# Optimization experiments

Measured on AMD Instinct MI355X. Metric: run time of the kernel, lower is better.

Reference implementation:

```python
import jax, jax.numpy as jnp
import numpy as np

THRESH = 0.3
OUT_THRESH = 0.3
LENS = 0.5  # surrogate-gradient window (ActFun in snn-delays repo)


@jax.custom_vjp
def spike(x):
    # Heaviside spike with rectangular surrogate gradient
    return (x > 0.0).astype(x.dtype)

def _spike_fwd(x):
    return spike(x), x

def _spike_bwd(x, g):
    return (g * (jnp.abs(x) < LENS).astype(g.dtype),)

spike.defvjp(_spike_fwd, _spike_bwd)


def setup_inputs() -> dict:
    key = jax.random.key(0)
    ks = jax.random.split(key, 7)
    B, T, I, H, O = 256, 50, 1024, 2048, 20
    # binary input spikes (rate ~0.2), as an SNN would receive
    inp = (jax.random.uniform(ks[0], (B, T, I)) < 0.2).astype(jnp.float32)
    # Linear(in, out, bias=False) -> weight [out, in], Kaiming-uniform-ish init
    w_ih = jax.random.uniform(ks[1], (H, I), minval=-1.0, maxval=1.0) / np.sqrt(I)
    w_hh = jax.random.uniform(ks[2], (H, H), minval=-1.0, maxval=1.0) / np.sqrt(H)
    w_ho = jax.random.uniform(ks[3], (O, H), minval=-1.0, maxval=1.0) / np.sqrt(H)
    tau_m_h = 0.83 + 0.1 * jax.random.normal(ks[4], (H,))
    tau_m_o = 0.83 + 0.1 * jax.random.normal(ks[5], (O,))
    return {"input": inp, "w_ih": w_ih, "w_hh": w_hh, "w_ho": w_ho,
            "tau_m_h": tau_m_h, "tau_m_o": tau_m_o}


def _rsnn_forward(inp, w_ih, w_hh, w_ho, tau_m_h, tau_m_o):
    B, T, I = inp.shape
    H = w_ih.shape[0]
    O = w_ho.shape[0]
    alpha_h = jnp.exp(-1.0 / tau_m_h)  # [H]
    alpha_o = jnp.exp(-1.0 / tau_m_o)  # [O]
    zH = jnp.zeros((B, H), inp.dtype)
    zO = jnp.zeros((B, O), inp.dtype)

    def step(carry, x_t):
        h_mem, h_spk, o_mem, o_spk, o_sum, mot = carry
        # hidden membrane update: input + recurrent + decayed (reset-gated) mem
        h_mem = (x_t @ w_ih.T) + (h_spk @ w_hh.T) + h_mem * alpha_h * (1.0 - h_spk)
        h_spk = spike(h_mem - THRESH)
        # output membrane update
        o_mem = o_mem * alpha_o * (1.0 - o_spk) + h_spk @ w_ho.T
        o_spk = spike(o_mem - OUT_THRESH)
        o_sum = o_sum + o_spk
        mot = mot + jax.nn.softmax(o_mem, axis=1)
        return (h_mem, h_spk, o_mem, o_spk, o_sum, mot), None

    init = (zH, zH, zO, zO, zO, zO)
    (h_mem, h_spk, o_mem, o_spk, o_sum, mot), _ = jax.lax.scan(
        step, init, jnp.swapaxes(inp, 0, 1))  # scan over time [T,B,I]
    return o_sum / T, mot


def reference(input, w_ih, w_hh, w_ho, tau_m_h, tau_m_o):
    return _rsnn_forward(input, w_ih, w_hh, w_ho, tau_m_h, tau_m_o)
```

## Files before the change

### kernel.cpp

```cpp
#include <hip/hip_runtime.h>
#include <stdint.h>
#include <math.h>


#define B_   256
#define T_   50
#define I_   1024
#define H_   2048
#define O_   20
#define XIN_T  262144
#define XS_BUF 524288
#define WNT 294912
#define WPL 98304

typedef __attribute__((ext_vector_type(4))) int intx4;
typedef long long ll_t;

__device__ __forceinline__ int digit_of(float v, int p) {
  int W = (int)rintf(v * 134217728.0f);
  int c0 = ((W + 128) & 255) - 128;
  int W1 = (W - c0) >> 8;
  int c1 = ((W1 + 128) & 255) - 128;
  int W2 = (W1 - c1) >> 8;
  return (p == 0) ? c0 : (p == 1) ? c1 : W2;
}

__global__ void prep_w(const float* __restrict__ w_ih,
                       const float* __restrict__ w_hh,
                       int8_t* __restrict__ Wtl) {
  int blk = blockIdx.x;
  int n = blk / 9, kg = blk % 9;
  int k9 = (kg * 256 + (int)threadIdx.x) * 4;
  int p = k9 / 3072, kk = k9 % 3072;
  const float* src = (kk < 1024) ? (w_ih + n * I_ + kk)
                                 : (w_hh + n * H_ + (kk - 1024));
  float4 v = *(const float4*)src;
  int d0 = digit_of(v.x, p) & 255;
  int d1 = digit_of(v.y, p) & 255;
  int d2 = digit_of(v.z, p) & 255;
  int d3 = digit_of(v.w, p) & 255;
  int packed = d0 | (d1 << 8) | (d2 << 16) | (d3 << 24);
  size_t off = (size_t)(n >> 5) * WNT + (size_t)p * WPL + (kk >> 6) * 2048 +
               (n & 31) * 64 + (kk & 63);
  *(int*)(Wtl + off) = packed;
}

__global__ void init_k(int8_t* __restrict__ Xin, int8_t* __restrict__ Xs,
                       float* __restrict__ Hm, const float* __restrict__ input,
                       const float* __restrict__ tau_h,
                       const float* __restrict__ tau_o,
                       float* __restrict__ AlphaH, float* __restrict__ AlphaO,
                       const float* __restrict__ w_ho, double* __restrict__ WhoD,
                       float* __restrict__ Om, float* __restrict__ Osp,
                       float* __restrict__ Osu, float* __restrict__ Mo) {
  int id = blockIdx.x * 256 + threadIdx.x;
  {
    int b = id >> 8, i4 = (id & 255) * 4;
    for (int t = 0; t < T_; ++t) {
      float4 v = *(const float4*)(input + ((size_t)(b * T_ + t) << 10) + i4);
      uchar4 pk;
      pk.x = v.x > 0.5f ? 1 : 0;
      pk.y = v.y > 0.5f ? 1 : 0;
      pk.z = v.z > 0.5f ? 1 : 0;
      pk.w = v.w > 0.5f ? 1 : 0;
      *(uchar4*)(Xin + (size_t)t * XIN_T + (b >> 6) * 65536 + (i4 >> 6) * 4096 +
                 (b & 63) * 64 + (i4 & 63)) = pk;
    }
  }
  *(double*)(Xs + (size_t)id * 8) = 0.0;
  *(float4*)(Hm + (size_t)id * 8) = make_float4(0.f, 0.f, 0.f, 0.f);
  *(float4*)(Hm + (size_t)id * 8 + 4) = make_float4(0.f, 0.f, 0.f, 0.f);
  if (id < 64 * O_ * 32) {
    int nt = id / 640, rem = id % 640, o = rem / 32, hl = rem & 31;
    WhoD[id] = (double)w_ho[o * H_ + nt * 32 + hl];
  }
  if (id < H_) AlphaH[id] = (float)exp((double)(-1.0f / tau_h[id]));
  if (id < O_) AlphaO[id] = (float)exp((double)(-1.0f / tau_o[id]));
  if (id < B_ * O_) {
    Om[id] = 0.f; Osp[id] = 0.f; Osu[id] = 0.f; Mo[id] = 0.f;
  }
}

__global__ __launch_bounds__(512, 2) void step_k(
    const int8_t* __restrict__ Wtl, const int8_t* __restrict__ Xin,
    int8_t* __restrict__ Xs, float* __restrict__ Hm, double* __restrict__ Po,
    const double* __restrict__ WhoD, const float* __restrict__ AlphaH,
    const float* __restrict__ AlphaO, float* __restrict__ Om,
    float* __restrict__ Osp, float* __restrict__ Osu, float* __restrict__ Mo,
    int t) {
  __shared__ double WhoL[640];
  __shared__ __align__(16) int8_t red[98304];
  __shared__ int8_t spk_lT[2048];

  const int j = blockIdx.x;
  const int nt = (j & 7) * 8 + ((j >> 3) & 7);
  const int mg = j >> 6;
  const int tid = threadIdx.x;
  const int l = tid & 63, k = tid >> 6;
  const int r_ = l & 15, q = l >> 4;

  for (int i = tid; i < 640; i += 512) WhoL[i] = WhoD[nt * 640 + i];

  const int8_t* Ain = Xin + (size_t)t * XIN_T + mg * 65536 + r_ * 64 + q * 16;
  const int8_t* Asp = Xs + (size_t)(t & 1) * XS_BUF + mg * 131072 + r_ * 64 + q * 16;
  const int8_t* Bw = Wtl + (size_t)nt * WNT + r_ * 64 + q * 16;
  const int u0 = k * 6;

  intx4 acc[4][2][3];
#pragma unroll
  for (int fr = 0; fr < 4; ++fr)
#pragma unroll
    for (int fc = 0; fc < 2; ++fc)
#pragma unroll
      for (int p = 0; p < 3; ++p) acc[fr][fc][p] = (intx4){0, 0, 0, 0};

  intx4 a[2][4], b[2][2][3];
  {
    const int8_t* ap = (u0 < 16) ? (Ain + u0 * 4096) : (Asp + (u0 - 16) * 4096);
#pragma unroll
    for (int fr = 0; fr < 4; ++fr) a[0][fr] = *(const intx4*)(ap + fr * 1024);
    const int8_t* bp = Bw + u0 * 2048;
#pragma unroll
    for (int p = 0; p < 3; ++p)
#pragma unroll
      for (int fc = 0; fc < 2; ++fc)
        b[0][fc][p] = *(const intx4*)(bp + p * WPL + fc * 1024);
  }
#pragma unroll
  for (int i = 0; i < 6; ++i) {
    const int cur = i & 1, nxt = cur ^ 1;
    if (i < 5) {
      const int un = u0 + i + 1;
      const int8_t* ap = (un < 16) ? (Ain + un * 4096) : (Asp + (un - 16) * 4096);
#pragma unroll
      for (int fr = 0; fr < 4; ++fr) a[nxt][fr] = *(const intx4*)(ap + fr * 1024);
      const int8_t* bp = Bw + un * 2048;
#pragma unroll
      for (int p = 0; p < 3; ++p)
#pragma unroll
        for (int fc = 0; fc < 2; ++fc)
          b[nxt][fc][p] = *(const intx4*)(bp + p * WPL + fc * 1024);
    }
#pragma unroll
    for (int fr = 0; fr < 4; ++fr)
#pragma unroll
      for (int fc = 0; fc < 2; ++fc)
#pragma unroll
        for (int p = 0; p < 3; ++p)
          acc[fr][fc][p] = __builtin_amdgcn_mfma_i32_16x16x64_i8(
              a[cur][fr], b[cur][fc][p], acc[fr][fc][p], 0, 0, 0);
  }

#define REDP(w, idx) (red + (((w) * 12 + (idx)) * 64 + l) * 16)

  int8_t* Xw = Xs + (size_t)((t + 1) & 1) * XS_BUF;
  auto epilogue = [&](intx4 s0, intx4 s1, intx4 s2, int fr_e, int fc_e) {
    const int h = nt * 32 + fc_e * 16 + r_;
    const float alpha = AlphaH[h];
    unsigned spkpack = 0;
#pragma unroll
    for (int jj = 0; jj < 4; ++jj) {
      ll_t Sv = (ll_t)s0[jj] + ((ll_t)s1[jj] << 8) + ((ll_t)s2[jj] << 16);
      float M = (float)((double)Sv * 7.450580596923828125e-9);
      const int brl = fr_e * 16 + q * 4 + jj;
      const int idx = (mg * 64 + brl) * H_ + h;
      float hp = Hm[idx];
      float spf = (hp - 0.3f) > 0.f ? 1.f : 0.f;
      float hm = M + hp * alpha * (1.0f - spf);
      Hm[idx] = hm;
      unsigned spk = (hm - 0.3f) > 0.f ? 1u : 0u;
      Xw[mg * 131072 + (h >> 6) * 4096 + brl * 64 + (h & 63)] = (int8_t)spk;
      spkpack |= spk << (8 * jj);
    }
    *(unsigned*)(spk_lT + (fc_e * 16 + r_) * 64 + fr_e * 16 + q * 4) = spkpack;
  };

#pragma unroll
  for (int fr = 0; fr < 2; ++fr)
#pragma unroll
    for (int fc = 0; fc < 2; ++fc)
#pragma unroll
      for (int p = 0; p < 3; ++p)
        *(intx4*)REDP(k, (fr * 2 + fc) * 3 + p) = acc[fr][fc][p];
  __syncthreads();
  if (k < 4) {
    const int fr_e = k >> 1, fc_e = k & 1;
    const int base = (fr_e * 2 + fc_e) * 3;
    intx4 s0 = (intx4){0, 0, 0, 0}, s1 = s0, s2 = s0;
#pragma unroll
    for (int w = 0; w < 8; ++w) {
      s0 = s0 + *(const intx4*)REDP(w, base + 0);
      s1 = s1 + *(const intx4*)REDP(w, base + 1);
      s2 = s2 + *(const intx4*)REDP(w, base + 2);
    }
    epilogue(s0, s1, s2, fr_e, fc_e);
  }
  __syncthreads();
#pragma unroll
  for (int fr = 0; fr < 2; ++fr)
#pragma unroll
    for (int fc = 0; fc < 2; ++fc)
#pragma unroll
      for (int p = 0; p < 3; ++p)
        *(intx4*)REDP(k, (fr * 2 + fc) * 3 + p) = acc[2 + fr][fc][p];
  __syncthreads();
  if (k >= 4) {
    const int fr_e = 2 + ((k - 4) >> 1), fc_e = k & 1;
    const int base = ((fr_e - 2) * 2 + fc_e) * 3;
    intx4 s0 = (intx4){0, 0, 0, 0}, s1 = s0, s2 = s0;
#pragma unroll
    for (int w = 0; w < 8; ++w) {
      s0 = s0 + *(const intx4*)REDP(w, base + 0);
      s1 = s1 + *(const intx4*)REDP(w, base + 1);
      s2 = s2 + *(const intx4*)REDP(w, base + 2);
    }
    epilogue(s0, s1, s2, fr_e, fc_e);
  }
  __syncthreads();

  if (tid < 256) {
    const int bl = tid >> 2, og = (tid & 3) * 5;
    const double* W0 = WhoL + og * 32;
    double a0 = 0, a1 = 0, a2 = 0, a3 = 0, a4 = 0;
#pragma unroll
    for (int hl = 0; hl < 32; ++hl) {
      double m = (double)spk_lT[hl * 64 + bl];
      a0 += m * W0[hl];
      a1 += m * W0[32 + hl];
      a2 += m * W0[64 + hl];
      a3 += m * W0[96 + hl];
      a4 += m * W0[128 + hl];
    }
    double* dst =
        Po + ((size_t)((t & 1) * 256 + mg * 64 + bl) * 64 + nt) * 20 + og;
    dst[0] = a0; dst[1] = a1; dst[2] = a2; dst[3] = a3; dst[4] = a4;
  } else if (k == 7 && t > 0) {
    float m = -3.0e38f;
    if (l < 20) {
      const double* pp = Po + ((size_t)(((t - 1) & 1) * 256 + j) * 64) * 20 + l;
      double s = 0.0;
#pragma unroll
      for (int n2 = 0; n2 < 64; ++n2) s += pp[n2 * 20];
      m = Om[j * O_ + l] * AlphaO[l] * (1.0f - Osp[j * O_ + l]) + (float)s;
    }
    float mx = m;
#pragma unroll
    for (int off = 16; off > 0; off >>= 1)
      mx = fmaxf(mx, __shfl_xor(mx, off, 32));
    float eo = (l < 20) ? expf(m - mx) : 0.f;
    float se = eo;
#pragma unroll
    for (int off = 16; off > 0; off >>= 1) se += __shfl_xor(se, off, 32);
    if (l < 20) {
      float sp = (m - 0.3f) > 0.f ? 1.f : 0.f;
      Om[j * O_ + l] = m;
      Osp[j * O_ + l] = sp;
      Osu[j * O_ + l] += sp;
      Mo[j * O_ + l] += eo / se;
    }
  }
#undef REDP
}

__global__ void final_k(const double* __restrict__ Po,
                        const float* __restrict__ AlphaO,
                        const float* __restrict__ Om,
                        const float* __restrict__ Osp,
                        const float* __restrict__ Osu,
                        const float* __restrict__ Mo, float* __restrict__ out) {
  __shared__ float om_l[O_];
  const int j = blockIdx.x, tid = threadIdx.x;
  if (tid < O_) {
    const double* pp = Po + ((size_t)(256 + j) * 64) * 20 + tid;
    double s = 0.0;
#pragma unroll
    for (int n2 = 0; n2 < 64; ++n2) s += pp[n2 * 20];
    float r = (float)s;
    float m = Om[j * O_ + tid] * AlphaO[tid] * (1.0f - Osp[j * O_ + tid]) + r;
    om_l[tid] = m;
  }
  __syncthreads();
  if (tid < O_) {
    float m = om_l[tid];
    float mx = om_l[0];
#pragma unroll
    for (int o = 1; o < O_; ++o) mx = fmaxf(mx, om_l[o]);
    float se = 0.f;
#pragma unroll
    for (int o = 0; o < O_; ++o) se += expf(om_l[o] - mx);
    float sp = (m - 0.3f) > 0.f ? 1.f : 0.f;
    out[j * O_ + tid] = (Osu[j * O_ + tid] + sp) / 50.0f;
    out[B_ * O_ + j * O_ + tid] = Mo[j * O_ + tid] + expf(m - mx) / se;
  }
}

extern "C" void kernel_launch(void* const* d_in, const int* in_sizes, int n_in,
                              void* d_out, int out_size, void* d_ws, size_t ws_size,
                              hipStream_t stream) {
  const float* input = (const float*)d_in[0];
  const float* w_ih  = (const float*)d_in[1];
  const float* w_hh  = (const float*)d_in[2];
  const float* w_ho  = (const float*)d_in[3];
  const float* tau_h = (const float*)d_in[4];
  const float* tau_o = (const float*)d_in[5];

  char* ws = (char*)d_ws;
  int8_t* Wtl    = (int8_t*)(ws);
  int8_t* Xin    = (int8_t*)(ws + 18874368);
  int8_t* Xs     = (int8_t*)(ws + 31981568);
  double* Po     = (double*)(ws + 33030144);
  float*  Hm     = (float*)(ws + 38273024);
  double* WhoD   = (double*)(ws + 40370176);
  float*  AlphaH = (float*)(ws + 40697856);
  float*  AlphaO = (float*)(ws + 40706048);
  float*  Om     = (float*)(ws + 40706176);
  float*  Osp    = (float*)(ws + 40726656);
  float*  Osu    = (float*)(ws + 40747136);
  float*  Mo     = (float*)(ws + 40767616);
  float*  out    = (float*)d_out;

  prep_w<<<2048 * 9, 256, 0, stream>>>(w_ih, w_hh, Wtl);
  init_k<<<256, 256, 0, stream>>>(Xin, Xs, Hm, input, tau_h, tau_o, AlphaH,
                                  AlphaO, w_ho, WhoD, Om, Osp, Osu, Mo);
  for (int t = 0; t < T_; ++t) {
    step_k<<<256, 512, 0, stream>>>(Wtl, Xin, Xs, Hm, Po, WhoD, AlphaH, AlphaO,
                                    Om, Osp, Osu, Mo, t);
  }
  final_k<<<256, 64, 0, stream>>>(Po, AlphaO, Om, Osp, Osu, Mo, out);
}
```

Baseline: 900.8 us.

## Fuse all timesteps into one persistent cooperative kernel with register-resident state

Replaces the 50 per-timestep launches and the final kernel with a single cooperative kernel that loops over time and uses grid.sync between steps. Each block keeps its weight slice in registers for the whole run (breg) and holds the hidden membrane and output state in registers instead of global memory, which removes the per-step weight reloads and the Hm/Om round trips. In exchange it pays a grid-wide barrier per step and much higher register pressure, which could cause spills or lower occupancy, and it requires all 256 blocks to be resident at once.

After: 3.207 ms. 3.56x slower.

```diff
diff --git a/kernel.cpp b/kernel.cpp
--- a/kernel.cpp
+++ b/kernel.cpp
@@ -1,6 +1,9 @@
 #include <hip/hip_runtime.h>
+#include <hip/hip_cooperative_groups.h>
 #include <stdint.h>
 #include <math.h>
+
+namespace cg = cooperative_groups;
 
 
 #define B_   256
@@ -46,13 +49,12 @@
 }
 
 __global__ void init_k(int8_t* __restrict__ Xin, int8_t* __restrict__ Xs,
-                       float* __restrict__ Hm, const float* __restrict__ input,
+                       const float* __restrict__ input,
                        const float* __restrict__ tau_h,
                        const float* __restrict__ tau_o,
                        float* __restrict__ AlphaH, float* __restrict__ AlphaO,
-                       const float* __restrict__ w_ho, double* __restrict__ WhoD,
-                       float* __restrict__ Om, float* __restrict__ Osp,
-                       float* __restrict__ Osu, float* __restrict__ Mo) {
+                       const float* __restrict__ w_ho,
+                       double* __restrict__ WhoD) {
   int id = blockIdx.x * 256 + threadIdx.x;
   {
     int b = id >> 8, i4 = (id & 255) * 4;
@@ -68,26 +70,20 @@
     }
   }
   *(double*)(Xs + (size_t)id * 8) = 0.0;
-  *(float4*)(Hm + (size_t)id * 8) = make_float4(0.f, 0.f, 0.f, 0.f);
-  *(float4*)(Hm + (size_t)id * 8 + 4) = make_float4(0.f, 0.f, 0.f, 0.f);
   if (id < 64 * O_ * 32) {
     int nt = id / 640, rem = id % 640, o = rem / 32, hl = rem & 31;
     WhoD[id] = (double)w_ho[o * H_ + nt * 32 + hl];
   }
   if (id < H_) AlphaH[id] = (float)exp((double)(-1.0f / tau_h[id]));
   if (id < O_) AlphaO[id] = (float)exp((double)(-1.0f / tau_o[id]));
-  if (id < B_ * O_) {
-    Om[id] = 0.f; Osp[id] = 0.f; Osu[id] = 0.f; Mo[id] = 0.f;
-  }
-}
-
-__global__ __launch_bounds__(512, 2) void step_k(
+}
+
+__global__ __launch_bounds__(512, 2) void rsnn_k(
     const int8_t* __restrict__ Wtl, const int8_t* __restrict__ Xin,
-    int8_t* __restrict__ Xs, float* __restrict__ Hm, double* __restrict__ Po,
+    int8_t* __restrict__ Xs, double* __restrict__ Po,
     const double* __restrict__ WhoD, const float* __restrict__ AlphaH,
-    const float* __restrict__ AlphaO, float* __restrict__ Om,
-    float* __restrict__ Osp, float* __restrict__ Osu, float* __restrict__ Mo,
-    int t) {
+    const float* __restrict__ AlphaO, float* __restrict__ out) {
+  cg::grid_group grid = cg::this_grid();
   __shared__ double WhoL[640];
   __shared__ __align__(16) int8_t red[98304];
   __shared__ int8_t spk_lT[2048];
@@ -101,197 +97,181 @@
 
   for (int i = tid; i < 640; i += 512) WhoL[i] = WhoD[nt * 640 + i];
 
-  const int8_t* Ain = Xin + (size_t)t * XIN_T + mg * 65536 + r_ * 64 + q * 16;
-  const int8_t* Asp = Xs + (size_t)(t & 1) * XS_BUF + mg * 131072 + r_ * 64 + q * 16;
+  const int fr_e = (k < 4) ? (k >> 1) : (2 + ((k - 4) >> 1));
+  const int fc_e = k & 1;
+  const int h_e = nt * 32 + fc_e * 16 + r_;
+  const float alpha_e = AlphaH[h_e];
+  const float alphaO_r = (l < O_) ? AlphaO[l] : 0.f;
+
+  float hm[4] = {0.f, 0.f, 0.f, 0.f};
+  float om = 0.f, osp = 0.f, osu = 0.f, mo = 0.f;
+
+  const int u0 = k * 6;
   const int8_t* Bw = Wtl + (size_t)nt * WNT + r_ * 64 + q * 16;
-  const int u0 = k * 6;
-
-  intx4 acc[4][2][3];
-#pragma unroll
-  for (int fr = 0; fr < 4; ++fr)
-#pragma unroll
-    for (int fc = 0; fc < 2; ++fc)
-#pragma unroll
-      for (int p = 0; p < 3; ++p) acc[fr][fc][p] = (intx4){0, 0, 0, 0};
-
-  intx4 a[2][4], b[2][2][3];
-  {
-    const int8_t* ap = (u0 < 16) ? (Ain + u0 * 4096) : (Asp + (u0 - 16) * 4096);
-#pragma unroll
-    for (int fr = 0; fr < 4; ++fr) a[0][fr] = *(const intx4*)(ap + fr * 1024);
-    const int8_t* bp = Bw + u0 * 2048;
+  intx4 breg[6][2][3];
+#pragma unroll
+  for (int i = 0; i < 6; ++i)
 #pragma unroll
     for (int p = 0; p < 3; ++p)
 #pragma unroll
       for (int fc = 0; fc < 2; ++fc)
-        b[0][fc][p] = *(const intx4*)(bp + p * WPL + fc * 1024);
-  }
-#pragma unroll
-  for (int i = 0; i < 6; ++i) {
-    const int cur = i & 1, nxt = cur ^ 1;
-    if (i < 5) {
-      const int un = u0 + i + 1;
-      const int8_t* ap = (un < 16) ? (Ain + un * 4096) : (Asp + (un - 16) * 4096);
-#pragma unroll
-      for (int fr = 0; fr < 4; ++fr) a[nxt][fr] = *(const intx4*)(ap + fr * 1024);
-      const int8_t* bp = Bw + un * 2048;
-#pragma unroll
-      for (int p = 0; p < 3; ++p)
+        breg[i][fc][p] =
+            *(const intx4*)(Bw + (size_t)(u0 + i) * 2048 + p * WPL + fc * 1024);
+
+  const int arow = r_ * 64 + q * 16;
+
+#define REDP(w, idx) (red + (((w) * 12 + (idx)) * 64 + l) * 16)
+
+  for (int t = 0; t <= T_; ++t) {
+    grid.sync();
+
+    if (t < T_) {
+      const int8_t* Ain = Xin + (size_t)t * XIN_T + mg * 65536 + arow;
+      const int8_t* Asp = Xs + (size_t)(t & 1) * XS_BUF + mg * 131072 + arow;
+      int8_t* Xw = Xs + (size_t)((t + 1) & 1) * XS_BUF;
+
+      intx4 acc[4][2][3];
+#pragma unroll
+      for (int fr = 0; fr < 4; ++fr)
 #pragma unroll
         for (int fc = 0; fc < 2; ++fc)
-          b[nxt][fc][p] = *(const intx4*)(bp + p * WPL + fc * 1024);
+#pragma unroll
+          for (int p = 0; p < 3; ++p) acc[fr][fc][p] = (intx4){0, 0, 0, 0};
+
+#pragma unroll
+      for (int i = 0; i < 6; ++i) {
+        const int u = u0 + i;
+        const int8_t* ap =
+            (u < 16) ? (Ain + u * 4096) : (Asp + (u - 16) * 4096);
+        intx4 a0 = *(const intx4*)ap;
+        intx4 a1 = *(const intx4*)(ap + 1024);
+        intx4 a2 = *(const intx4*)(ap + 2048);
+        intx4 a3 = *(const intx4*)(ap + 3072);
+#pragma unroll
+        for (int p = 0; p < 3; ++p)
+#pragma unroll
+          for (int fc = 0; fc < 2; ++fc) {
+            acc[0][fc][p] = __builtin_amdgcn_mfma_i32_16x16x64_i8(
+                a0, breg[i][fc][p], acc[0][fc][p], 0, 0, 0);
+            acc[1][fc][p] = __builtin_amdgcn_mfma_i32_16x16x64_i8(
+                a1, breg[i][fc][p], acc[1][fc][p], 0, 0, 0);
+            acc[2][fc][p] = __builtin_amdgcn_mfma_i32_16x16x64_i8(
+                a2, breg[i][fc][p], acc[2][fc][p], 0, 0, 0);
+            acc[3][fc][p] = __builtin_amdgcn_mfma_i32_16x16x64_i8(
+                a3, breg[i][fc][p], acc[3][fc][p], 0, 0, 0);
+          }
+      }
+
+      auto epilogue = [&](intx4 s0, intx4 s1, intx4 s2) {
+        unsigned spkpack = 0;
+#pragma unroll
+        for (int jj = 0; jj < 4; ++jj) {
+          ll_t Sv = (ll_t)s0[jj] + ((ll_t)s1[jj] << 8) + ((ll_t)s2[jj] << 16);
+          float M = (float)((double)Sv * 7.450580596923828125e-9);
+          float hp = hm[jj];
+          float spf = (hp - 0.3f) > 0.f ? 1.f : 0.f;
+          float hmn = M + hp * alpha_e * (1.0f - spf);
+          hm[jj] = hmn;
+          unsigned spk = (hmn - 0.3f) > 0.f ? 1u : 0u;
+          const int brl = fr_e * 16 + q * 4 + jj;
+          Xw[mg * 131072 + (h_e >> 6) * 4096 + brl * 64 + (h_e & 63)] =
+              (int8_t)spk;
+          spkpack |= spk << (8 * jj);
+        }
+        *(unsigned*)(spk_lT + (fc_e * 16 + r_) * 64 + fr_e * 16 + q * 4) =
+            spkpack;
+      };
+
+#pragma unroll
+      for (int fr = 0; fr < 2; ++fr)
+#pragma unroll
+        for (int fc = 0; fc < 2; ++fc)
+#pragma unroll
+          for (int p = 0; p < 3; ++p)
+            *(intx4*)REDP(k, (fr * 2 + fc) * 3 + p) = acc[fr][fc][p];
+      __syncthreads();
+      if (k < 4) {
+        const int base = (fr_e * 2 + fc_e) * 3;
+        intx4 s0 = (intx4){0, 0, 0, 0}, s1 = s0, s2 = s0;
+#pragma unroll
+        for (int w = 0; w < 8; ++w) {
+          s0 = s0 + *(const intx4*)REDP(w, base + 0);
+          s1 = s1 + *(const intx4*)REDP(w, base + 1);
+          s2 = s2 + *(const intx4*)REDP(w, base + 2);
+        }
+        epilogue(s0, s1, s2);
+      }
+      __syncthreads();
+#pragma unroll
+      for (int fr = 0; fr < 2; ++fr)
+#pragma unroll
+        for (int fc = 0; fc < 2; ++fc)
+#pragma unroll
+          for (int p = 0; p < 3; ++p)
+            *(intx4*)REDP(k, (fr * 2 + fc) * 3 + p) = acc[2 + fr][fc][p];
+      __syncthreads();
+      if (k >= 4) {
+        const int base = ((fr_e - 2) * 2 + fc_e) * 3;
+        intx4 s0 = (intx4){0, 0, 0, 0}, s1 = s0, s2 = s0;
+#pragma unroll
+        for (int w = 0; w < 8; ++w) {
+          s0 = s0 + *(const intx4*)REDP(w, base + 0);
+          s1 = s1 + *(const intx4*)REDP(w, base + 1);
+          s2 = s2 + *(const intx4*)REDP(w, base + 2);
+        }
+        epilogue(s0, s1, s2);
+      }
+      __syncthreads();
+
+      if (tid < 256) {
+        const int bl = tid >> 2, og = (tid & 3) * 5;
+        const double* W0 = WhoL + og * 32;
+        double a0 = 0, a1 = 0, a2 = 0, a3 = 0, a4 = 0;
+#pragma unroll
+        for (int hl = 0; hl < 32; ++hl) {
+          double m = (double)spk_lT[hl * 64 + bl];
+          a0 += m * W0[hl];
+          a1 += m * W0[32 + hl];
+          a2 += m * W0[64 + hl];
+          a3 += m * W0[96 + hl];
+          a4 += m * W0[128 + hl];
+        }
+        double* dst =
+            Po + ((size_t)((t & 1) * 256 + mg * 64 + bl) * 64 + nt) * 20 + og;
+        dst[0] = a0; dst[1] = a1; dst[2] = a2; dst[3] = a3; dst[4] = a4;
+      }
     }
-#pragma unroll
-    for (int fr = 0; fr < 4; ++fr)
-#pragma unroll
-      for (int fc = 0; fc < 2; ++fc)
-#pragma unroll
-        for (int p = 0; p < 3; ++p)
-          acc[fr][fc][p] = __builtin_amdgcn_mfma_i32_16x16x64_i8(
-              a[cur][fr], b[cur][fc][p], acc[fr][fc][p], 0, 0, 0);
-  }
-
-#define REDP(w, idx) (red + (((w) * 12 + (idx)) * 64 + l) * 16)
-
-  int8_t* Xw = Xs + (size_t)((t + 1) & 1) * XS_BUF;
-  auto epilogue = [&](intx4 s0, intx4 s1, intx4 s2, int fr_e, int fc_e) {
-    const int h = nt * 32 + fc_e * 16 + r_;
-    const float alpha = AlphaH[h];
-    unsigned spkpack = 0;
-#pragma unroll
-    for (int jj = 0; jj < 4; ++jj) {
-      ll_t Sv = (ll_t)s0[jj] + ((ll_t)s1[jj] << 8) + ((ll_t)s2[jj] << 16);
-      float M = (float)((double)Sv * 7.450580596923828125e-9);
-      const int brl = fr_e * 16 + q * 4 + jj;
-      const int idx = (mg * 64 + brl) * H_ + h;
-      float hp = Hm[idx];
-      float spf = (hp - 0.3f) > 0.f ? 1.f : 0.f;
-      float hm = M + hp * alpha * (1.0f - spf);
-      Hm[idx] = hm;
-      unsigned spk = (hm - 0.3f) > 0.f ? 1u : 0u;
-      Xw[mg * 131072 + (h >> 6) * 4096 + brl * 64 + (h & 63)] = (int8_t)spk;
-      spkpack |= spk << (8 * jj);
-    }
-    *(unsigned*)(spk_lT + (fc_e * 16 + r_) * 64 + fr_e * 16 + q * 4) = spkpack;
-  };
-
-#pragma unroll
-  for (int fr = 0; fr < 2; ++fr)
-#pragma unroll
-    for (int fc = 0; fc < 2; ++fc)
-#pragma unroll
-      for (int p = 0; p < 3; ++p)
-        *(intx4*)REDP(k, (fr * 2 + fc) * 3 + p) = acc[fr][fc][p];
-  __syncthreads();
-  if (k < 4) {
-    const int fr_e = k >> 1, fc_e = k & 1;
-    const int base = (fr_e * 2 + fc_e) * 3;
-    intx4 s0 = (intx4){0, 0, 0, 0}, s1 = s0, s2 = s0;
-#pragma unroll
-    for (int w = 0; w < 8; ++w) {
-      s0 = s0 + *(const intx4*)REDP(w, base + 0);
-      s1 = s1 + *(const intx4*)REDP(w, base + 1);
-      s2 = s2 + *(const intx4*)REDP(w, base + 2);
-    }
-    epilogue(s0, s1, s2, fr_e, fc_e);
-  }
-  __syncthreads();
-#pragma unroll
-  for (int fr = 0; fr < 2; ++fr)
-#pragma unroll
-    for (int fc = 0; fc < 2; ++fc)
-#pragma unroll
-      for (int p = 0; p < 3; ++p)
-        *(intx4*)REDP(k, (fr * 2 + fc) * 3 + p) = acc[2 + fr][fc][p];
-  __syncthreads();
-  if (k >= 4) {
-    const int fr_e = 2 + ((k - 4) >> 1), fc_e = k & 1;
-    const int base = ((fr_e - 2) * 2 + fc_e) * 3;
-    intx4 s0 = (intx4){0, 0, 0, 0}, s1 = s0, s2 = s0;
-#pragma unroll
-    for (int w = 0; w < 8; ++w) {
-      s0 = s0 + *(const intx4*)REDP(w, base + 0);
-      s1 = s1 + *(const intx4*)REDP(w, base + 1);
-      s2 = s2 + *(const intx4*)REDP(w, base + 2);
-    }
-    epilogue(s0, s1, s2, fr_e, fc_e);
-  }
-  __syncthreads();
-
-  if (tid < 256) {
-    const int bl = tid >> 2, og = (tid & 3) * 5;
-    const double* W0 = WhoL + og * 32;
-    double a0 = 0, a1 = 0, a2 = 0, a3 = 0, a4 = 0;
-#pragma unroll
-    for (int hl = 0; hl < 32; ++hl) {
-      double m = (double)spk_lT[hl * 64 + bl];
-      a0 += m * W0[hl];
-      a1 += m * W0[32 + hl];
-      a2 += m * W0[64 + hl];
-      a3 += m * W0[96 + hl];
-      a4 += m * W0[128 + hl];
-    }
-    double* dst =
-        Po + ((size_t)((t & 1) * 256 + mg * 64 + bl) * 64 + nt) * 20 + og;
-    dst[0] = a0; dst[1] = a1; dst[2] = a2; dst[3] = a3; dst[4] = a4;
-  } else if (k == 7 && t > 0) {
-    float m = -3.0e38f;
-    if (l < 20) {
-      const double* pp = Po + ((size_t)(((t - 1) & 1) * 256 + j) * 64) * 20 + l;
-      double s = 0.0;
-#pragma unroll
-      for (int n2 = 0; n2 < 64; ++n2) s += pp[n2 * 20];
-      m = Om[j * O_ + l] * AlphaO[l] * (1.0f - Osp[j * O_ + l]) + (float)s;
-    }
-    float mx = m;
-#pragma unroll
-    for (int off = 16; off > 0; off >>= 1)
-      mx = fmaxf(mx, __shfl_xor(mx, off, 32));
-    float eo = (l < 20) ? expf(m - mx) : 0.f;
-    float se = eo;
-#pragma unroll
-    for (int off = 16; off > 0; off >>= 1) se += __shfl_xor(se, off, 32);
-    if (l < 20) {
-      float sp = (m - 0.3f) > 0.f ? 1.f : 0.f;
-      Om[j * O_ + l] = m;
-      Osp[j * O_ + l] = sp;
-      Osu[j * O_ + l] += sp;
-      Mo[j * O_ + l] += eo / se;
+
+    if (k == 7 && t > 0) {
+      float m = -3.0e38f;
+      if (l < O_) {
+        const double* pp =
+            Po + ((size_t)(((t - 1) & 1) * 256 + j) * 64) * 20 + l;
+        double s = 0.0;
+#pragma unroll
+        for (int n2 = 0; n2 < 64; ++n2) s += pp[n2 * 20];
+        m = om * alphaO_r * (1.0f - osp) + (float)s;
+      }
+      float mx = m;
+#pragma unroll
+      for (int off = 16; off > 0; off >>= 1)
+        mx = fmaxf(mx, __shfl_xor(mx, off, 32));
+      float eo = (l < O_) ? expf(m - mx) : 0.f;
+      float se = eo;
+#pragma unroll
+      for (int off = 16; off > 0; off >>= 1) se += __shfl_xor(se, off, 32);
+      if (l < O_) {
+        float sp = (m - 0.3f) > 0.f ? 1.f : 0.f;
+        if (t < T_) {
+          om = m; osp = sp; osu += sp; mo += eo / se;
+        } else {
+          out[j * O_ + l] = (osu + sp) / 50.0f;
+          out[B_ * O_ + j * O_ + l] = mo + eo / se;
+        }
+      }
     }
   }
 #undef REDP
-}
-
-__global__ void final_k(const double* __restrict__ Po,
-                        const float* __restrict__ AlphaO,
-                        const float* __restrict__ Om,
-                        const float* __restrict__ Osp,
-                        const float* __restrict__ Osu,
-                        const float* __restrict__ Mo, float* __restrict__ out) {
-  __shared__ float om_l[O_];
-  const int j = blockIdx.x, tid = threadIdx.x;
-  if (tid < O_) {
-    const double* pp = Po + ((size_t)(256 + j) * 64) * 20 + tid;
-    double s = 0.0;
-#pragma unroll
-    for (int n2 = 0; n2 < 64; ++n2) s += pp[n2 * 20];
-    float r = (float)s;
-    float m = Om[j * O_ + tid] * AlphaO[tid] * (1.0f - Osp[j * O_ + tid]) + r;
-    om_l[tid] = m;
-  }
-  __syncthreads();
-  if (tid < O_) {
-    float m = om_l[tid];
-    float mx = om_l[0];
-#pragma unroll
-    for (int o = 1; o < O_; ++o) mx = fmaxf(mx, om_l[o]);
-    float se = 0.f;
-#pragma unroll
-    for (int o = 0; o < O_; ++o) se += expf(om_l[o] - mx);
-    float sp = (m - 0.3f) > 0.f ? 1.f : 0.f;
-    out[j * O_ + tid] = (Osu[j * O_ + tid] + sp) / 50.0f;
-    out[B_ * O_ + j * O_ + tid] = Mo[j * O_ + tid] + expf(m - mx) / se;
-  }
 }
 
 extern "C" void kernel_launch(void* const* d_in, const int* in_sizes, int n_in,
@@ -309,22 +289,16 @@
   int8_t* Xin    = (int8_t*)(ws + 18874368);
   int8_t* Xs     = (int8_t*)(ws + 31981568);
   double* Po     = (double*)(ws + 33030144);
-  float*  Hm     = (float*)(ws + 38273024);
   double* WhoD   = (double*)(ws + 40370176);
   float*  AlphaH = (float*)(ws + 40697856);
   float*  AlphaO = (float*)(ws + 40706048);
-  float*  Om     = (float*)(ws + 40706176);
-  float*  Osp    = (float*)(ws + 40726656);
-  float*  Osu    = (float*)(ws + 40747136);
-  float*  Mo     = (float*)(ws + 40767616);
   float*  out    = (float*)d_out;
 
   prep_w<<<2048 * 9, 256, 0, stream>>>(w_ih, w_hh, Wtl);
-  init_k<<<256, 256, 0, stream>>>(Xin, Xs, Hm, input, tau_h, tau_o, AlphaH,
-                                  AlphaO, w_ho, WhoD, Om, Osp, Osu, Mo);
-  for (int t = 0; t < T_; ++t) {
-    step_k<<<256, 512, 0, stream>>>(Wtl, Xin, Xs, Hm, Po, WhoD, AlphaH, AlphaO,
-                                    Om, Osp, Osu, Mo, t);
-  }
-  final_k<<<256, 64, 0, stream>>>(Po, AlphaO, Om, Osp, Osu, Mo, out);
-}
+  init_k<<<256, 256, 0, stream>>>(Xin, Xs, input, tau_h, tau_o, AlphaH,
+                                  AlphaO, w_ho, WhoD);
+  void* args[] = {(void*)&Wtl, (void*)&Xin, (void*)&Xs, (void*)&Po,
+                  (void*)&WhoD, (void*)&AlphaH, (void*)&AlphaO, (void*)&out};
+  hipLaunchCooperativeKernel((void*)rsnn_k, dim3(256), dim3(512), args, 0,
+                             stream);
+}
```
